# Performance work log

Hardware: AMD Instinct MI355X
Metric: run time of the kernel (lower is better)

## Reference

```python
import jax, jax.numpy as jnp
import numpy as np

N, E = 50000, 400000
IN_C, H, C = 128, 8, 16
NEG_SLOPE = 0.2


def setup_inputs() -> dict:
    key = jax.random.key(0)
    k1, k2, k3, k4 = jax.random.split(key, 4)
    x = jax.random.normal(k1, (N, IN_C), dtype=jnp.float32)
    edge_index = jax.random.randint(k2, (2, E), 0, N, dtype=jnp.int32)
    # Xavier-uniform linear weight [H*C, IN_C] (no bias in lin)
    lim_w = float(np.sqrt(6.0 / (IN_C + H * C)))
    W = jax.random.uniform(k3, (H * C, IN_C), dtype=jnp.float32, minval=-lim_w, maxval=lim_w)
    lim_a = float(np.sqrt(6.0 / (1 + 2 * C)))
    att = jax.random.uniform(k4, (1, H, 2 * C), dtype=jnp.float32, minval=-lim_a, maxval=lim_a)
    bias = jnp.zeros((H * C,), dtype=jnp.float32)
    return {"x": x, "edge_index": edge_index, "W": W, "att": att, "bias": bias}


def reference(x, edge_index, W, att, bias):
    n = x.shape[0]
    # linear projection -> [N, H, C]
    xt = (x @ W.T).reshape(n, H, C)
    # add self loops -> [2, E+N]
    loops = jnp.arange(n, dtype=edge_index.dtype)
    src = jnp.concatenate([edge_index[0], loops])
    tgt = jnp.concatenate([edge_index[1], loops])
    xs = xt[src]  # [Etot, H, C]
    xd = xt[tgt]  # [Etot, H, C]
    att_s, att_d = att[0, :, :C], att[0, :, C:]
    alpha = jnp.einsum('ehc,hc->eh', xs, att_s) + jnp.einsum('ehc,hc->eh', xd, att_d)
    alpha = jax.nn.leaky_relu(alpha, NEG_SLOPE)
    # segment softmax over edges sharing the same target node
    amax = jax.ops.segment_max(alpha, tgt, num_segments=n)  # [N, H]
    ex = jnp.exp(alpha - amax[tgt])
    denom = jax.ops.segment_sum(ex, tgt, num_segments=n)  # [N, H]
    alpha = ex / denom[tgt]
    # weighted scatter-add aggregation
    msgs = alpha[..., None] * xs  # [Etot, H, C]
    out = jax.ops.segment_sum(msgs, tgt, num_segments=n)  # [N, H, C]
    out = out.reshape(n, H * C) + bias
    return out
```

## Files before the change

### kernel.cpp

```cpp
#include <hip/hip_runtime.h>
#include <hip/hip_bf16.h>

typedef __attribute__((ext_vector_type(8))) short short8;
typedef __attribute__((ext_vector_type(4))) float f32x4;

#define SLOTS 64

static __device__ __forceinline__ float lrelu(float a) {
    return a > 0.0f ? a : 0.2f * a;
}
static __device__ __forceinline__ unsigned f2bf(float f) {
    unsigned u = __float_as_uint(f);
    return (u + 0x7fffu + ((u >> 16) & 1u)) >> 16;
}
static __device__ __forceinline__ float bf2f(unsigned b) {
    return __uint_as_float(b << 16);
}
static __device__ __forceinline__ unsigned pack2(float a, float b) {
    return f2bf(a) | (f2bf(b) << 16);
}

__global__ __launch_bounds__(256) void prep_B_kernel(
    const float* __restrict__ W, const float* __restrict__ att,
    unsigned* __restrict__ Bbu)
{
    int i = blockIdx.x * 256 + threadIdx.x;
    if (i < 8192) {
        Bbu[i] = pack2(W[2 * i], W[2 * i + 1]);
    } else if (i < 9216) {
        int e = (i - 8192) * 2;
        int r2 = e >> 7;
        int k = e & 127;
        int h = r2 & 7, sel = r2 >> 3;
        const float* ap = att + h * 32 + sel * 16;
        float v0 = 0.0f, v1 = 0.0f;
        for (int c = 0; c < 16; c++) {
            float a = ap[c];
            v0 = fmaf(a, W[(h * 16 + c) * 128 + k], v0);
            v1 = fmaf(a, W[(h * 16 + c) * 128 + k + 1], v1);
        }
        Bbu[i] = pack2(v0, v1);
    }
}

__global__ __launch_bounds__(256) void gemm_mfma_kernel(
    const float* __restrict__ x, const uint4* __restrict__ Bb4,
    unsigned short* __restrict__ xtb16, float* __restrict__ s,
    float* __restrict__ d, int n)
{
    __shared__ uint4 BbL[2304];
    const int t = threadIdx.x;
    for (int c = t; c < 2304; c += 256) {
        int j = c >> 4, kc = c & 15;
        BbL[(j << 4) | (kc ^ (j & 15))] = Bb4[c];
    }
    __syncthreads();

    const int lane = t & 63;
    const int wid = t >> 6;
    const int l15 = lane & 15, lhi = lane >> 4;
    const int row0 = blockIdx.x * 64 + wid * 16;
    const int arow = min(row0 + l15, n - 1);
    const float4* xv = (const float4*)(x + (size_t)arow * 128);

    float4 A0[4], A1[4];
    #pragma unroll
    for (int ks = 0; ks < 4; ks++) {
        A0[ks] = xv[ks * 8 + lhi * 2];
        A1[ks] = xv[ks * 8 + lhi * 2 + 1];
    }

    f32x4 acc[9];
    #pragma unroll
    for (int ct = 0; ct < 9; ct++) acc[ct] = (f32x4){0.f, 0.f, 0.f, 0.f};

    #pragma unroll
    for (int ks = 0; ks < 4; ks++) {
        union { unsigned u[4]; short8 v; } af;
        af.u[0] = pack2(A0[ks].x, A0[ks].y);
        af.u[1] = pack2(A0[ks].z, A0[ks].w);
        af.u[2] = pack2(A1[ks].x, A1[ks].y);
        af.u[3] = pack2(A1[ks].z, A1[ks].w);
        const int kc = ks * 4 + lhi;
        #pragma unroll
        for (int ct = 0; ct < 9; ct++) {
            const int j = ct * 16 + l15;
            union { uint4 q; short8 v; } bfr;
            bfr.q = BbL[(j << 4) | (kc ^ (j & 15))];
            acc[ct] = __builtin_amdgcn_mfma_f32_16x16x32_bf16(af.v, bfr.v, acc[ct], 0, 0, 0);
        }
    }

    #pragma unroll
    for (int r = 0; r < 4; r++) {
        const int row = row0 + lhi * 4 + r;
        if (row < n) {
            #pragma unroll
            for (int ct = 0; ct < 8; ct++)
                xtb16[(size_t)row * 128 + ct * 16 + l15] =
                    (unsigned short)f2bf(acc[ct][r]);
            const float v = acc[8][r];
            if (l15 < 8) s[row * 8 + l15] = v;
            else         d[row * 8 + (l15 - 8)] = v;
        }
    }
}

__global__ __launch_bounds__(256) void zero4_kernel(int4* __restrict__ p, int n4)
{
    int i = blockIdx.x * 256 + threadIdx.x;
    if (i < n4) p[i] = make_int4(0, 0, 0, 0);
}

__global__ void scatter_direct_kernel(
    const int* __restrict__ ei, int* __restrict__ cnt,
    int* __restrict__ srcs, int E)
{
    int e = blockIdx.x * 256 + threadIdx.x;
    if (e < E) {
        int tgt = ei[E + e];
        int pos = atomicAdd(&cnt[tgt], 1);
        if (pos < SLOTS) srcs[(size_t)tgt * SLOTS + pos] = ei[e];
    }
}

__global__ __launch_bounds__(256) void aggregate_kernel(
    const unsigned* __restrict__ xtb, const float* __restrict__ s,
    const float* __restrict__ d, const int* __restrict__ cnt,
    const int* __restrict__ srcs, const float* __restrict__ bias,
    float* __restrict__ out, int n)
{
    const int wid = (blockIdx.x * 256 + threadIdx.x) >> 6;
    const int lane = threadIdx.x & 63;
    if (wid >= n) return;
    const int node = wid;
    const int off = node * SLOTS;
    const int deg = min(cnt[node], SLOTS);
    const int hB = lane >> 3;
    const float dB = d[node * 8 + hB];
    const float2 bv = ((const float2*)bias)[lane];

    const float svn = s[node * 8 + hB];
    const unsigned un = xtb[(size_t)node * 64 + lane];

    int ia0 = (0 < deg) ? srcs[off + 0] : node;
    int ia1 = (1 < deg) ? srcs[off + 1] : node;
    int ia2 = (2 < deg) ? srcs[off + 2] : node;
    int ia3 = (3 < deg) ? srcs[off + 3] : node;
    int ib0 = (4 < deg) ? srcs[off + 4] : node;
    int ib1 = (5 < deg) ? srcs[off + 5] : node;
    int ib2 = (6 < deg) ? srcs[off + 6] : node;
    int ib3 = (7 < deg) ? srcs[off + 7] : node;
    float sa0 = s[ia0 * 8 + hB], sa1 = s[ia1 * 8 + hB];
    float sa2 = s[ia2 * 8 + hB], sa3 = s[ia3 * 8 + hB];
    unsigned ua0 = xtb[(size_t)ia0 * 64 + lane];
    unsigned ua1 = xtb[(size_t)ia1 * 64 + lane];
    unsigned ua2 = xtb[(size_t)ia2 * 64 + lane];
    unsigned ua3 = xtb[(size_t)ia3 * 64 + lane];

    const float w_self = __expf(lrelu(svn + dB));
    float wsum = w_self;
    float accx = w_self * bf2f(un & 0xffffu);
    float accy = w_self * bf2f(un >> 16);

    for (int e = 0; e < deg; e += 4) {
        const int ic0 = (e + 8 < deg) ? srcs[off + e + 8] : node;
        const int ic1 = (e + 9 < deg) ? srcs[off + e + 9] : node;
        const int ic2 = (e + 10 < deg) ? srcs[off + e + 10] : node;
        const int ic3 = (e + 11 < deg) ? srcs[off + e + 11] : node;
        const float sb0 = s[ib0 * 8 + hB], sb1 = s[ib1 * 8 + hB];
        const float sb2 = s[ib2 * 8 + hB], sb3 = s[ib3 * 8 + hB];
        const unsigned ub0 = xtb[(size_t)ib0 * 64 + lane];
        const unsigned ub1 = xtb[(size_t)ib1 * 64 + lane];
        const unsigned ub2 = xtb[(size_t)ib2 * 64 + lane];
        const unsigned ub3 = xtb[(size_t)ib3 * 64 + lane];
        const float w0 = (e + 0 < deg) ? __expf(lrelu(sa0 + dB)) : 0.0f;
        const float w1 = (e + 1 < deg) ? __expf(lrelu(sa1 + dB)) : 0.0f;
        const float w2 = (e + 2 < deg) ? __expf(lrelu(sa2 + dB)) : 0.0f;
        const float w3 = (e + 3 < deg) ? __expf(lrelu(sa3 + dB)) : 0.0f;
        wsum += (w0 + w1) + (w2 + w3);
        accx = fmaf(w0, bf2f(ua0 & 0xffffu), accx);
        accy = fmaf(w0, bf2f(ua0 >> 16), accy);
        accx = fmaf(w1, bf2f(ua1 & 0xffffu), accx);
        accy = fmaf(w1, bf2f(ua1 >> 16), accy);
        accx = fmaf(w2, bf2f(ua2 & 0xffffu), accx);
        accy = fmaf(w2, bf2f(ua2 >> 16), accy);
        accx = fmaf(w3, bf2f(ua3 & 0xffffu), accx);
        accy = fmaf(w3, bf2f(ua3 >> 16), accy);
        sa0 = sb0; sa1 = sb1; sa2 = sb2; sa3 = sb3;
        ua0 = ub0; ua1 = ub1; ua2 = ub2; ua3 = ub3;
        ib0 = ic0; ib1 = ic1; ib2 = ic2; ib3 = ic3;
    }
    const float inv = 1.0f / wsum;
    ((float2*)out)[(size_t)node * 64 + lane] =
        make_float2(fmaf(accx, inv, bv.x), fmaf(accy, inv, bv.y));
}

extern "C" void kernel_launch(void* const* d_in, const int* in_sizes, int n_in,
                              void* d_out, int out_size, void* d_ws, size_t ws_size,
                              hipStream_t stream)
{
    const float* x    = (const float*)d_in[0];
    const int*   ei   = (const int*)d_in[1];
    const float* W    = (const float*)d_in[2];
    const float* att  = (const float*)d_in[3];
    const float* bias = (const float*)d_in[4];
    float* out = (float*)d_out;

    const int n = in_sizes[0] / 128;
    const int E = in_sizes[1] / 2;

    const size_t cnt_pad = ((size_t)n + 3) & ~(size_t)3;
    const size_t need_bytes =
        (size_t)n * 64 * sizeof(unsigned) +
        (size_t)n * 16 * sizeof(float) +
        (cnt_pad + (size_t)n * SLOTS + 9216) * sizeof(int);
    if (ws_size < need_bytes) return;

    unsigned* xtb = (unsigned*)d_ws;
    float* s  = (float*)(xtb + (size_t)n * 64);
    float* d  = s + (size_t)n * 8;
    int* cnt  = (int*)(d + (size_t)n * 8);
    int* srcs = cnt + cnt_pad;
    unsigned* Bbu = (unsigned*)(srcs + (size_t)n * SLOTS);

    const int n4 = (int)(cnt_pad / 4);
    prep_B_kernel<<<dim3(36), dim3(256), 0, stream>>>(W, att, Bbu);
    gemm_mfma_kernel<<<dim3((n + 63) / 64), dim3(256), 0, stream>>>(
        x, (const uint4*)Bbu, (unsigned short*)xtb, s, d, n);
    zero4_kernel<<<dim3((n4 + 255) / 256), dim3(256), 0, stream>>>((int4*)cnt, n4);
    scatter_direct_kernel<<<dim3((E + 255) / 256), dim3(256), 0, stream>>>(ei, cnt, srcs, E);
    aggregate_kernel<<<dim3((n + 3) / 4), dim3(256), 0, stream>>>(
        xtb, s, d, cnt, srcs, bias, out, n);
}
```

Measured before the change: 74.00 us.

## Split aggregate wave into two edge halves and fuse count zeroing into prep

The aggregate kernel now splits each wavefront into two 32-lane halves. Each half handles alternate edges of the node using 8-byte bf16 loads covering four channels per lane. The halves are combined with a cross-half shuffle before a float4 output store. This gives two independent gather streams per node and wider loads, aiming to raise memory-level parallelism for low-degree nodes. Zeroing the counts is also folded into the prep kernel launch, removing one kernel launch.

```diff
diff --git a/kernel.cpp b/kernel.cpp
--- a/kernel.cpp
+++ b/kernel.cpp
@@ -20,11 +20,16 @@
     return f2bf(a) | (f2bf(b) << 16);
 }
 
-__global__ __launch_bounds__(256) void prep_B_kernel(
+__global__ __launch_bounds__(256) void zero_prep_kernel(
     const float* __restrict__ W, const float* __restrict__ att,
-    unsigned* __restrict__ Bbu)
-{
-    int i = blockIdx.x * 256 + threadIdx.x;
+    unsigned* __restrict__ Bbu, int4* __restrict__ cnt4, int n4, int nZero)
+{
+    if ((int)blockIdx.x < nZero) {
+        int i = blockIdx.x * 256 + threadIdx.x;
+        if (i < n4) cnt4[i] = make_int4(0, 0, 0, 0);
+        return;
+    }
+    int i = (blockIdx.x - nZero) * 256 + threadIdx.x;
     if (i < 8192) {
         Bbu[i] = pack2(W[2 * i], W[2 * i + 1]);
     } else if (i < 9216) {
@@ -106,12 +111,6 @@
     }
 }
 
-__global__ __launch_bounds__(256) void zero4_kernel(int4* __restrict__ p, int n4)
-{
-    int i = blockIdx.x * 256 + threadIdx.x;
-    if (i < n4) p[i] = make_int4(0, 0, 0, 0);
-}
-
 __global__ void scatter_direct_kernel(
     const int* __restrict__ ei, int* __restrict__ cnt,
     int* __restrict__ srcs, int E)
@@ -136,64 +135,91 @@
     const int node = wid;
     const int off = node * SLOTS;
     const int deg = min(cnt[node], SLOTS);
-    const int hB = lane >> 3;
+    const int half = lane >> 5;
+    const int sl = lane & 31;
+    const int hB = sl >> 2;
     const float dB = d[node * 8 + hB];
-    const float2 bv = ((const float2*)bias)[lane];
+    const uint2* xt2 = (const uint2*)xtb;
 
     const float svn = s[node * 8 + hB];
-    const unsigned un = xtb[(size_t)node * 64 + lane];
-
-    int ia0 = (0 < deg) ? srcs[off + 0] : node;
-    int ia1 = (1 < deg) ? srcs[off + 1] : node;
-    int ia2 = (2 < deg) ? srcs[off + 2] : node;
-    int ia3 = (3 < deg) ? srcs[off + 3] : node;
-    int ib0 = (4 < deg) ? srcs[off + 4] : node;
-    int ib1 = (5 < deg) ? srcs[off + 5] : node;
-    int ib2 = (6 < deg) ? srcs[off + 6] : node;
-    int ib3 = (7 < deg) ? srcs[off + 7] : node;
+    const uint2 un = xt2[(size_t)node * 32 + sl];
+
+    const int h0 = half;
+    int ia0 = (h0 + 0  < deg) ? srcs[off + h0 + 0]  : node;
+    int ia1 = (h0 + 2  < deg) ? srcs[off + h0 + 2]  : node;
+    int ia2 = (h0 + 4  < deg) ? srcs[off + h0 + 4]  : node;
+    int ia3 = (h0 + 6  < deg) ? srcs[off + h0 + 6]  : node;
+    int ib0 = (h0 + 8  < deg) ? srcs[off + h0 + 8]  : node;
+    int ib1 = (h0 + 10 < deg) ? srcs[off + h0 + 10] : node;
+    int ib2 = (h0 + 12 < deg) ? srcs[off + h0 + 12] : node;
+    int ib3 = (h0 + 14 < deg) ? srcs[off + h0 + 14] : node;
     float sa0 = s[ia0 * 8 + hB], sa1 = s[ia1 * 8 + hB];
     float sa2 = s[ia2 * 8 + hB], sa3 = s[ia3 * 8 + hB];
-    unsigned ua0 = xtb[(size_t)ia0 * 64 + lane];
-    unsigned ua1 = xtb[(size_t)ia1 * 64 + lane];
-    unsigned ua2 = xtb[(size_t)ia2 * 64 + lane];
-    unsigned ua3 = xtb[(size_t)ia3 * 64 + lane];
-
-    const float w_self = __expf(lrelu(svn + dB));
-    float wsum = w_self;
-    float accx = w_self * bf2f(un & 0xffffu);
-    float accy = w_self * bf2f(un >> 16);
-
-    for (int e = 0; e < deg; e += 4) {
-        const int ic0 = (e + 8 < deg) ? srcs[off + e + 8] : node;
-        const int ic1 = (e + 9 < deg) ? srcs[off + e + 9] : node;
-        const int ic2 = (e + 10 < deg) ? srcs[off + e + 10] : node;
-        const int ic3 = (e + 11 < deg) ? srcs[off + e + 11] : node;
+    uint2 ua0 = xt2[(size_t)ia0 * 32 + sl];
+    uint2 ua1 = xt2[(size_t)ia1 * 32 + sl];
+    uint2 ua2 = xt2[(size_t)ia2 * 32 + sl];
+    uint2 ua3 = xt2[(size_t)ia3 * 32 + sl];
+
+    float wsum = 0.0f, a0 = 0.0f, a1 = 0.0f, a2 = 0.0f, a3 = 0.0f;
+    if (half == 0) {
+        const float ws = __expf(lrelu(svn + dB));
+        wsum = ws;
+        a0 = ws * bf2f(un.x & 0xffffu);
+        a1 = ws * bf2f(un.x >> 16);
+        a2 = ws * bf2f(un.y & 0xffffu);
+        a3 = ws * bf2f(un.y >> 16);
+    }
+
+    for (int e8 = 0; e8 < deg; e8 += 8) {
+        const int p = off + h0 + e8 + 16;
+        const int ic0 = (h0 + e8 + 16 < deg) ? srcs[p + 0] : node;
+        const int ic1 = (h0 + e8 + 18 < deg) ? srcs[p + 2] : node;
+        const int ic2 = (h0 + e8 + 20 < deg) ? srcs[p + 4] : node;
+        const int ic3 = (h0 + e8 + 22 < deg) ? srcs[p + 6] : node;
         const float sb0 = s[ib0 * 8 + hB], sb1 = s[ib1 * 8 + hB];
         const float sb2 = s[ib2 * 8 + hB], sb3 = s[ib3 * 8 + hB];
-        const unsigned ub0 = xtb[(size_t)ib0 * 64 + lane];
-        const unsigned ub1 = xtb[(size_t)ib1 * 64 + lane];
-        const unsigned ub2 = xtb[(size_t)ib2 * 64 + lane];
-        const unsigned ub3 = xtb[(size_t)ib3 * 64 + lane];
-        const float w0 = (e + 0 < deg) ? __expf(lrelu(sa0 + dB)) : 0.0f;
-        const float w1 = (e + 1 < deg) ? __expf(lrelu(sa1 + dB)) : 0.0f;
-        const float w2 = (e + 2 < deg) ? __expf(lrelu(sa2 + dB)) : 0.0f;
-        const float w3 = (e + 3 < deg) ? __expf(lrelu(sa3 + dB)) : 0.0f;
+        const uint2 ub0 = xt2[(size_t)ib0 * 32 + sl];
+        const uint2 ub1 = xt2[(size_t)ib1 * 32 + sl];
+        const uint2 ub2 = xt2[(size_t)ib2 * 32 + sl];
+        const uint2 ub3 = xt2[(size_t)ib3 * 32 + sl];
+        const float w0 = (h0 + e8 + 0 < deg) ? __expf(lrelu(sa0 + dB)) : 0.0f;
+        const float w1 = (h0 + e8 + 2 < deg) ? __expf(lrelu(sa1 + dB)) : 0.0f;
+        const float w2 = (h0 + e8 + 4 < deg) ? __expf(lrelu(sa2 + dB)) : 0.0f;
+        const float w3 = (h0 + e8 + 6 < deg) ? __expf(lrelu(sa3 + dB)) : 0.0f;
         wsum += (w0 + w1) + (w2 + w3);
-        accx = fmaf(w0, bf2f(ua0 & 0xffffu), accx);
-        accy = fmaf(w0, bf2f(ua0 >> 16), accy);
-        accx = fmaf(w1, bf2f(ua1 & 0xffffu), accx);
-        accy = fmaf(w1, bf2f(ua1 >> 16), accy);
-        accx = fmaf(w2, bf2f(ua2 & 0xffffu), accx);
-        accy = fmaf(w2, bf2f(ua2 >> 16), accy);
-        accx = fmaf(w3, bf2f(ua3 & 0xffffu), accx);
-        accy = fmaf(w3, bf2f(ua3 >> 16), accy);
+        a0 = fmaf(w0, bf2f(ua0.x & 0xffffu), a0);
+        a1 = fmaf(w0, bf2f(ua0.x >> 16), a1);
+        a2 = fmaf(w0, bf2f(ua0.y & 0xffffu), a2);
+        a3 = fmaf(w0, bf2f(ua0.y >> 16), a3);
+        a0 = fmaf(w1, bf2f(ua1.x & 0xffffu), a0);
+        a1 = fmaf(w1, bf2f(ua1.x >> 16), a1);
+        a2 = fmaf(w1, bf2f(ua1.y & 0xffffu), a2);
+        a3 = fmaf(w1, bf2f(ua1.y >> 16), a3);
+        a0 = fmaf(w2, bf2f(ua2.x & 0xffffu), a0);
+        a1 = fmaf(w2, bf2f(ua2.x >> 16), a1);
+        a2 = fmaf(w2, bf2f(ua2.y & 0xffffu), a2);
+        a3 = fmaf(w2, bf2f(ua2.y >> 16), a3);
+        a0 = fmaf(w3, bf2f(ua3.x & 0xffffu), a0);
+        a1 = fmaf(w3, bf2f(ua3.x >> 16), a1);
+        a2 = fmaf(w3, bf2f(ua3.y & 0xffffu), a2);
+        a3 = fmaf(w3, bf2f(ua3.y >> 16), a3);
         sa0 = sb0; sa1 = sb1; sa2 = sb2; sa3 = sb3;
         ua0 = ub0; ua1 = ub1; ua2 = ub2; ua3 = ub3;
         ib0 = ic0; ib1 = ic1; ib2 = ic2; ib3 = ic3;
     }
-    const float inv = 1.0f / wsum;
-    ((float2*)out)[(size_t)node * 64 + lane] =
-        make_float2(fmaf(accx, inv, bv.x), fmaf(accy, inv, bv.y));
+
+    wsum += __shfl_xor(wsum, 32);
+    a0 += __shfl_xor(a0, 32);
+    a1 += __shfl_xor(a1, 32);
+    a2 += __shfl_xor(a2, 32);
+    a3 += __shfl_xor(a3, 32);
+    if (half == 0) {
+        const float inv = 1.0f / wsum;
+        const float4 b4 = ((const float4*)bias)[sl];
+        ((float4*)out)[(size_t)node * 32 + sl] =
+            make_float4(fmaf(a0, inv, b4.x), fmaf(a1, inv, b4.y),
+                        fmaf(a2, inv, b4.z), fmaf(a3, inv, b4.w));
+    }
 }
 
 extern "C" void kernel_launch(void* const* d_in, const int* in_sizes, int n_in,
@@ -225,10 +251,11 @@
     unsigned* Bbu = (unsigned*)(srcs + (size_t)n * SLOTS);
 
     const int n4 = (int)(cnt_pad / 4);
-    prep_B_kernel<<<dim3(36), dim3(256), 0, stream>>>(W, att, Bbu);
+    const int nZero = (n4 + 255) / 256;
+    zero_prep_kernel<<<dim3(nZero + 36), dim3(256), 0, stream>>>(
+        W, att, Bbu, (int4*)cnt, n4, nZero);
     gemm_mfma_kernel<<<dim3((n + 63) / 64), dim3(256), 0, stream>>>(
         x, (const uint4*)Bbu, (unsigned short*)xtb, s, d, n);
-    zero4_kernel<<<dim3((n4 + 255) / 256), dim3(256), 0, stream>>>((int4*)cnt, n4);
     scatter_direct_kernel<<<dim3((E + 255) / 256), dim3(256), 0, stream>>>(ei, cnt, srcs, E);
     aggregate_kernel<<<dim3((n + 3) / 4), dim3(256), 0, stream>>>(
         xtb, s, d, cnt, srcs, bias, out, n);
```

After: 73.46 us. Within noise of the previous version (-0.7%).
